# Kernel optimization log

Hardware: AMD Instinct MI355X
Metric: run time of the kernel (lower is better)

Reference implementation:

```python
import jax, jax.numpy as jnp
import numpy as np

B, C, K, P, STRIDE, ITERS = 32, 32, 3, 4, 1, 3
PSIZE = P * P
EPS = 1e-6


def unfold_patches(x, K, stride):
    # Replicates F.unfold(x_chw, kernel_size=K, padding=K//2, stride=stride)
    # followed by transpose(1,2).view(b, oh, ow, K*K, c) — including the
    # channel-major flat ordering that the view reinterprets.
    b, h, w, c = x.shape
    pad = K // 2
    xp = jnp.pad(jnp.transpose(x, (0, 3, 1, 2)), ((0, 0), (0, 0), (pad, pad), (pad, pad)))
    oh = (h + 2 * pad - K) // stride + 1
    ow = (w + 2 * pad - K) // stride + 1
    rows = []
    for ki in range(K):
        cols = []
        for kj in range(K):
            cols.append(xp[:, :, ki:ki + (oh - 1) * stride + 1:stride, kj:kj + (ow - 1) * stride + 1:stride])
        rows.append(jnp.stack(cols, axis=2))  # (b, c, K, oh, ow)
    pat = jnp.stack(rows, axis=2)  # (b, c, K, K, oh, ow)
    pat = pat.reshape(b, c * K * K, oh * ow)  # unfold output (b, c*K*K, L)
    pat = jnp.transpose(pat, (0, 2, 1)).reshape(b, oh, ow, K * K, c)
    return pat, oh, ow


def squash(s, eps=EPS):
    s2 = jnp.sum(s * s, axis=-1, keepdims=True)
    return (s2 / (1.0 + s2)) * s / jnp.sqrt(s2 + eps)


def dynamic_routing(v, a_in, iters=ITERS, eps=EPS):
    # v: (n, in_votes, C, psize), a_in: (n, in_votes, 1)
    n, in_votes, Cc, _ = v.shape
    b_ij = jnp.zeros((n, in_votes, Cc), dtype=v.dtype)
    a_in = jnp.clip(a_in, 0.0001, 1.0)
    v_j = None
    for t in range(iters):
        c_ij = jax.nn.softmax(b_ij, axis=2) * a_in
        c_ij = c_ij / (jnp.sum(c_ij, axis=2, keepdims=True) + eps)
        s_j = jnp.einsum('nic,nicq->ncq', c_ij, v)
        v_j = squash(s_j)
        if t < iters - 1:
            agreement = jnp.einsum('nicq,ncq->nic', v, v_j)
            b_ij = b_ij + agreement
    a_out = jnp.clip(jnp.sqrt(jnp.sum(v_j * v_j, axis=-1) + eps), 0.0001, 1.0 - 0.0001)
    return v_j, a_out


def setup_inputs() -> dict:
    key = jax.random.key(0)
    k1, k2 = jax.random.split(key)
    x = jax.random.normal(k1, (2, 14, 14, B * (PSIZE + 1)), dtype=jnp.float32)
    weights = jax.random.normal(k2, (K * K * B, C, PSIZE, PSIZE), dtype=jnp.float32) * 0.02
    return {"x": x, "weights": weights}


def reference(x, weights):
    b, h, w, c = x.shape
    patches, oh, ow = unfold_patches(x, K, STRIDE)
    p_in = patches[..., :B * PSIZE].reshape(b * oh * ow, K * K * B, PSIZE)
    a_in = patches[..., B * PSIZE:].reshape(b * oh * ow, K * K * B, 1)
    votes = jnp.einsum('bip,icpq->bicq', p_in, weights)  # (n, KKB, C, psize)
    p_vec, a_vec = dynamic_routing(votes, a_in)
    p_out = p_vec.reshape(b, oh, ow, C * PSIZE)
    a_out = a_vec.reshape(b, oh, ow, C)
    out = jnp.concatenate([p_out, a_out], axis=3)
    p_out = jnp.nan_to_num(p_out, nan=0.0, posinf=10000.0, neginf=-10000.0)
    a_out = jnp.nan_to_num(a_out, nan=0.5, posinf=1.0 - 0.0001, neginf=0.0001)
    out = jnp.nan_to_num(out, nan=0.0, posinf=10000.0, neginf=-10000.0)
    return p_out, a_out, out
```

## Files before the change

kernel.cpp:

```cpp
#include <hip/hip_runtime.h>
#include <hip/hip_fp16.h>
#include <math.h>

#define NB 392
#define NI 288
#define NC 32
#define NQ 16
#define CQ 512
#define CH 544
#define EPSV 1e-6f

#define VSCALE 32.0f
#define VINV (1.0f / 32.0f)

#define OFF_AOUT 200704
#define OFF_CAT  213248

#define RT_THREADS 512
#define RT_WAVES 8

typedef _Float16 v4h __attribute__((ext_vector_type(4)));
typedef float v4f __attribute__((ext_vector_type(4)));
typedef float v2f __attribute__((ext_vector_type(2)));

__device__ __forceinline__ float gather_x(const float* __restrict__ x, int n, int j) {
    int c_idx = j / 9;
    int rem = j - c_idx * 9;
    int ki = rem / 3;
    int kj = rem - ki * 3;
    int b_ = n / 196;
    int rest = n - b_ * 196;
    int yy = rest / 14;
    int xx = rest - yy * 14;
    int iy = yy + ki - 1;
    int ix = xx + kj - 1;
    float v = 0.f;
    if ((unsigned)iy < 14u && (unsigned)ix < 14u)
        v = x[((b_ * 14 + iy) * 14 + ix) * CH + c_idx];
    return v;
}

__global__ __launch_bounds__(256) void votes_k(const float* __restrict__ x,
                                               const float* __restrict__ wts,
                                               uchar* __restrict__ votes) {
    __shared__ uint tile[64 * 36];
    int mtt = blockIdx.x;
    int i = blockIdx.y;
    int t = threadIdx.x;
    int wv = t >> 6;
    int l = t & 63;
    int col = l & 15;
    int quad = l >> 4;

    int n_row = mtt * 64 + wv * 16 + col;
    v4h av = {};
    if (n_row < NB) {
        int jb = (i >> 5) * CH + (i & 31) * 16 + quad * 4;
#pragma unroll
        for (int kk = 0; kk < 4; ++kk)
            av[kk] = (_Float16)gather_x(x, n_row, jb + kk);
    }

    const float* wb = wts + (size_t)i * 8192 + quad * 64 + col;
    const uchar* tileb = (const uchar*)tile;

    for (int ch = 0; ch < 4; ++ch) {
#pragma unroll
        for (int c8 = 0; c8 < 8; ++c8) {
            int ct = ch * 8 + c8;
            const float* wp = wb + ct * 256;
            v4h bv;
            bv[0] = (_Float16)wp[0];
            bv[1] = (_Float16)wp[16];
            bv[2] = (_Float16)wp[32];
            bv[3] = (_Float16)wp[48];
            v4f acc = {0.f, 0.f, 0.f, 0.f};
            acc = __builtin_amdgcn_mfma_f32_16x16x16f16(bv, av, acc, 0, 0, 0);
            uint u = __builtin_amdgcn_cvt_pk_fp8_f32(acc[0] * VSCALE, acc[1] * VSCALE, 0, false);
            u = __builtin_amdgcn_cvt_pk_fp8_f32(acc[2] * VSCALE, acc[3] * VSCALE, u, true);
            tile[(wv * 16 + col) * 36 + c8 * 4 + quad] = u;
        }
        __syncthreads();
#pragma unroll
        for (int k = 0; k < 2; ++k) {
            int idx = k * 256 + t;
            int row = idx >> 3;
            int off = idx & 7;
            int n_out = mtt * 64 + row;
            if (n_out < NB) {
                uint4 d = *(const uint4*)&tileb[row * 144 + off * 16];
                *(uint4*)(votes + (((size_t)n_out * NI + i) << 9) + ch * 128 + off * 16) = d;
            }
        }
        __syncthreads();
    }
}

__global__ __launch_bounds__(RT_THREADS) void routing_k(const uchar* __restrict__ votes,
                                                        const float* __restrict__ x,
                                                        float* __restrict__ out) {
    __shared__ float afs[NI];
    __shared__ float sred[RT_WAVES * CQ];
    __shared__ float vj[CQ];
    __shared__ float aout_s[NC];

    int n = blockIdx.x;
    int t = threadIdx.x;
    int wv = t >> 6;
    int l = t & 63;
    int c = l & 31;
    int g = l >> 5;

    if (t < NI) {
        int j = (t >> 5) * CH + 512 + (t & 31);
        float v = gather_x(x, n, j);
        float a = fminf(fmaxf(v, 1e-4f), 1.0f);
        afs[t] = a / (a + EPSV);
    }
    __syncthreads();

    const uchar* vb = votes + (size_t)n * NI * 512;
    float vjr[16];
    float sreg[16];

#define VROW(S) (((const uint4*)(vb + ((size_t)(((((S) << 3) + wv) << 1) + g) << 9)))[c])

    for (int iter = 0; iter < 3; ++iter) {
#pragma unroll
        for (int q = 0; q < 16; ++q) sreg[q] = 0.f;

        uint4 f0 = VROW(0), f1 = VROW(1), f2 = VROW(2), f3 = VROW(3);

#pragma clang loop unroll_count(2)
        for (int s = 0; s < 18; ++s) {
            int i = ((s << 3) + wv) * 2 + g;
            uint4 cur = f0;
            f0 = f1; f1 = f2; f2 = f3;
            if (s + 4 < 18) f3 = VROW(s + 4);

            float vt[16];
            {
                v2f p;
                p = __builtin_amdgcn_cvt_pk_f32_fp8(cur.x, false); vt[0] = p[0];  vt[1] = p[1];
                p = __builtin_amdgcn_cvt_pk_f32_fp8(cur.x, true);  vt[2] = p[0];  vt[3] = p[1];
                p = __builtin_amdgcn_cvt_pk_f32_fp8(cur.y, false); vt[4] = p[0];  vt[5] = p[1];
                p = __builtin_amdgcn_cvt_pk_f32_fp8(cur.y, true);  vt[6] = p[0];  vt[7] = p[1];
                p = __builtin_amdgcn_cvt_pk_f32_fp8(cur.z, false); vt[8] = p[0];  vt[9] = p[1];
                p = __builtin_amdgcn_cvt_pk_f32_fp8(cur.z, true);  vt[10] = p[0]; vt[11] = p[1];
                p = __builtin_amdgcn_cvt_pk_f32_fp8(cur.w, false); vt[12] = p[0]; vt[13] = p[1];
                p = __builtin_amdgcn_cvt_pk_f32_fp8(cur.w, true);  vt[14] = p[0]; vt[15] = p[1];
            }
            float cij;
            if (iter == 0) {
                cij = afs[i] * (1.0f / 32.0f);
            } else {
                float ah = 0.f;
#pragma unroll
                for (int q = 0; q < 16; ++q) ah += vt[q] * vjr[q];
                float e = __expf(ah);
                float ssum = e;
                ssum += __shfl_xor(ssum, 1);
                ssum += __shfl_xor(ssum, 2);
                ssum += __shfl_xor(ssum, 4);
                ssum += __shfl_xor(ssum, 8);
                ssum += __shfl_xor(ssum, 16);
                cij = e * __builtin_amdgcn_rcpf(ssum) * afs[i];
            }
#pragma unroll
            for (int q = 0; q < 16; ++q) sreg[q] += cij * vt[q];
        }

#pragma unroll
        for (int q = 0; q < 16; ++q) sreg[q] += __shfl_xor(sreg[q], 32);
        if (g == 0) {
            float* sw = &sred[wv * CQ + c];
#pragma unroll
            for (int q = 0; q < 16; ++q) sw[q * 32] = sreg[q];
        }
        __syncthreads();
        {
            float ssum = 0.f;
#pragma unroll
            for (int k = 0; k < RT_WAVES; ++k) ssum += sred[k * CQ + t];
            sred[t] = ssum * VINV;
        }
        __syncthreads();

        if (t < NC) {
            float s2 = 0.f;
#pragma unroll
            for (int q = 0; q < 16; ++q) {
                float s = sred[q * 32 + t];
                s2 += s * s;
            }
            float f = (s2 / (1.f + s2)) / sqrtf(s2 + EPSV);
            float vn2 = 0.f;
#pragma unroll
            for (int q = 0; q < 16; ++q) {
                float v = f * sred[q * 32 + t];
                vj[q * 32 + t] = v;
                vn2 += v * v;
            }
            if (iter == 2) {
                float ao = sqrtf(vn2 + EPSV);
                ao = fminf(fmaxf(ao, 1e-4f), 1.f - 1e-4f);
                aout_s[t] = ao;
            }
        }
        __syncthreads();
        if (iter < 2) {
#pragma unroll
            for (int q = 0; q < 16; ++q) {
                float v = vj[q * 32 + c] * VINV;
                vjr[q] = (iter == 0) ? v : vjr[q] + v;
            }
        }
    }

    {
        float v = vj[(t & 15) * 32 + (t >> 4)];
        out[(size_t)n * CQ + t] = v;
        out[OFF_CAT + (size_t)n * 544 + t] = v;
    }
    if (t < NC) {
        float ao = aout_s[t];
        out[OFF_AOUT + n * 32 + t] = ao;
        out[OFF_CAT + (size_t)n * 544 + 512 + t] = ao;
    }
}

extern "C" void kernel_launch(void* const* d_in, const int* in_sizes, int n_in,
                              void* d_out, int out_size, void* d_ws, size_t ws_size,
                              hipStream_t stream) {
    const float* x = (const float*)d_in[0];
    const float* wts = (const float*)d_in[1];
    float* out = (float*)d_out;
    uchar* votes = (uchar*)d_ws;

    hipLaunchKernelGGL(votes_k, dim3(7, NI), dim3(256), 0, stream,
                       x, wts, votes);
    hipLaunchKernelGGL(routing_k, dim3(NB), dim3(RT_THREADS), 0, stream,
                       votes, x, out);
}
```

Baseline: 115.3 us.

## Cache per-capsule fp8 votes in LDS for later routing iterations

In the routing kernel, the first iteration writes each block's fp8 vote rows (288x512 bytes) into shared memory as it streams them from global memory. Iterations two and three then read votes from LDS instead of refetching them from global memory or L2. To fit the roughly 144KB cache, the cross-wave reduction buffer is halved and the reduction is split into two phases with an extra barrier. The block now uses almost all of the CU's LDS, which limits occupancy to one 512-thread block per CU.

```diff
diff --git a/kernel.cpp b/kernel.cpp
--- a/kernel.cpp
+++ b/kernel.cpp
@@ -17,7 +17,6 @@
 #define OFF_CAT  213248
 
 #define RT_THREADS 512
-#define RT_WAVES 8
 
 typedef _Float16 v4h __attribute__((ext_vector_type(4)));
 typedef float v4f __attribute__((ext_vector_type(4)));
@@ -99,9 +98,10 @@
 __global__ __launch_bounds__(RT_THREADS) void routing_k(const uchar* __restrict__ votes,
                                                         const float* __restrict__ x,
                                                         float* __restrict__ out) {
+    __shared__ uint4 vlds4[NI * 32];
+    __shared__ float sred[4 * CQ];
+    __shared__ float vj[CQ];
     __shared__ float afs[NI];
-    __shared__ float sred[RT_WAVES * CQ];
-    __shared__ float vj[CQ];
     __shared__ float aout_s[NC];
 
     int n = blockIdx.x;
@@ -125,63 +125,35 @@
 
 #define VROW(S) (((const uint4*)(vb + ((size_t)(((((S) << 3) + wv) << 1) + g) << 9)))[c])
 
-    for (int iter = 0; iter < 3; ++iter) {
-#pragma unroll
-        for (int q = 0; q < 16; ++q) sreg[q] = 0.f;
-
-        uint4 f0 = VROW(0), f1 = VROW(1), f2 = VROW(2), f3 = VROW(3);
-
-#pragma clang loop unroll_count(2)
-        for (int s = 0; s < 18; ++s) {
-            int i = ((s << 3) + wv) * 2 + g;
-            uint4 cur = f0;
-            f0 = f1; f1 = f2; f2 = f3;
-            if (s + 4 < 18) f3 = VROW(s + 4);
-
-            float vt[16];
-            {
-                v2f p;
-                p = __builtin_amdgcn_cvt_pk_f32_fp8(cur.x, false); vt[0] = p[0];  vt[1] = p[1];
-                p = __builtin_amdgcn_cvt_pk_f32_fp8(cur.x, true);  vt[2] = p[0];  vt[3] = p[1];
-                p = __builtin_amdgcn_cvt_pk_f32_fp8(cur.y, false); vt[4] = p[0];  vt[5] = p[1];
-                p = __builtin_amdgcn_cvt_pk_f32_fp8(cur.y, true);  vt[6] = p[0];  vt[7] = p[1];
-                p = __builtin_amdgcn_cvt_pk_f32_fp8(cur.z, false); vt[8] = p[0];  vt[9] = p[1];
-                p = __builtin_amdgcn_cvt_pk_f32_fp8(cur.z, true);  vt[10] = p[0]; vt[11] = p[1];
-                p = __builtin_amdgcn_cvt_pk_f32_fp8(cur.w, false); vt[12] = p[0]; vt[13] = p[1];
-                p = __builtin_amdgcn_cvt_pk_f32_fp8(cur.w, true);  vt[14] = p[0]; vt[15] = p[1];
-            }
-            float cij;
-            if (iter == 0) {
-                cij = afs[i] * (1.0f / 32.0f);
-            } else {
-                float ah = 0.f;
-#pragma unroll
-                for (int q = 0; q < 16; ++q) ah += vt[q] * vjr[q];
-                float e = __expf(ah);
-                float ssum = e;
-                ssum += __shfl_xor(ssum, 1);
-                ssum += __shfl_xor(ssum, 2);
-                ssum += __shfl_xor(ssum, 4);
-                ssum += __shfl_xor(ssum, 8);
-                ssum += __shfl_xor(ssum, 16);
-                cij = e * __builtin_amdgcn_rcpf(ssum) * afs[i];
-            }
-#pragma unroll
-            for (int q = 0; q < 16; ++q) sreg[q] += cij * vt[q];
-        }
-
+#define DECODE(CUR, VT) { v2f p_; \
+    p_ = __builtin_amdgcn_cvt_pk_f32_fp8(CUR.x, false); VT[0] = p_[0];  VT[1] = p_[1]; \
+    p_ = __builtin_amdgcn_cvt_pk_f32_fp8(CUR.x, true);  VT[2] = p_[0];  VT[3] = p_[1]; \
+    p_ = __builtin_amdgcn_cvt_pk_f32_fp8(CUR.y, false); VT[4] = p_[0];  VT[5] = p_[1]; \
+    p_ = __builtin_amdgcn_cvt_pk_f32_fp8(CUR.y, true);  VT[6] = p_[0];  VT[7] = p_[1]; \
+    p_ = __builtin_amdgcn_cvt_pk_f32_fp8(CUR.z, false); VT[8] = p_[0];  VT[9] = p_[1]; \
+    p_ = __builtin_amdgcn_cvt_pk_f32_fp8(CUR.z, true);  VT[10] = p_[0]; VT[11] = p_[1]; \
+    p_ = __builtin_amdgcn_cvt_pk_f32_fp8(CUR.w, false); VT[12] = p_[0]; VT[13] = p_[1]; \
+    p_ = __builtin_amdgcn_cvt_pk_f32_fp8(CUR.w, true);  VT[14] = p_[0]; VT[15] = p_[1]; }
+
+    auto reduce_squash = [&](int iter) {
 #pragma unroll
         for (int q = 0; q < 16; ++q) sreg[q] += __shfl_xor(sreg[q], 32);
-        if (g == 0) {
+        if (g == 0 && wv < 4) {
             float* sw = &sred[wv * CQ + c];
 #pragma unroll
             for (int q = 0; q < 16; ++q) sw[q * 32] = sreg[q];
+        }
+        __syncthreads();
+        if (g == 0 && wv >= 4) {
+            float* sw = &sred[(wv - 4) * CQ + c];
+#pragma unroll
+            for (int q = 0; q < 16; ++q) sw[q * 32] += sreg[q];
         }
         __syncthreads();
         {
             float ssum = 0.f;
 #pragma unroll
-            for (int k = 0; k < RT_WAVES; ++k) ssum += sred[k * CQ + t];
+            for (int k = 0; k < 4; ++k) ssum += sred[k * CQ + t];
             sred[t] = ssum * VINV;
         }
         __syncthreads();
@@ -215,6 +187,59 @@
                 vjr[q] = (iter == 0) ? v : vjr[q] + v;
             }
         }
+    };
+
+    {
+#pragma unroll
+        for (int q = 0; q < 16; ++q) sreg[q] = 0.f;
+
+        uint4 f0 = VROW(0), f1 = VROW(1), f2 = VROW(2), f3 = VROW(3);
+
+#pragma clang loop unroll_count(2)
+        for (int s = 0; s < 18; ++s) {
+            int i = (s << 4) + (wv << 1) + g;
+            uint4 cur = f0;
+            f0 = f1; f1 = f2; f2 = f3;
+            if (s + 4 < 18) f3 = VROW(s + 4);
+
+            vlds4[i * 32 + c] = cur;
+
+            float vt[16];
+            DECODE(cur, vt);
+            float cij = afs[i] * (1.0f / 32.0f);
+#pragma unroll
+            for (int q = 0; q < 16; ++q) sreg[q] += cij * vt[q];
+        }
+        reduce_squash(0);
+    }
+
+    for (int iter = 1; iter < 3; ++iter) {
+#pragma unroll
+        for (int q = 0; q < 16; ++q) sreg[q] = 0.f;
+
+#pragma clang loop unroll_count(2)
+        for (int s = 0; s < 18; ++s) {
+            int i = (s << 4) + (wv << 1) + g;
+            uint4 cur = vlds4[i * 32 + c];
+
+            float vt[16];
+            DECODE(cur, vt);
+
+            float ah = 0.f;
+#pragma unroll
+            for (int q = 0; q < 16; ++q) ah += vt[q] * vjr[q];
+            float e = __expf(ah);
+            float ssum = e;
+            ssum += __shfl_xor(ssum, 1);
+            ssum += __shfl_xor(ssum, 2);
+            ssum += __shfl_xor(ssum, 4);
+            ssum += __shfl_xor(ssum, 8);
+            ssum += __shfl_xor(ssum, 16);
+            float cij = e * __builtin_amdgcn_rcpf(ssum) * afs[i];
+#pragma unroll
+            for (int q = 0; q < 16; ++q) sreg[q] += cij * vt[q];
+        }
+        reduce_squash(iter);
     }
 
     {
```

After: 124.2 us. 1.08x slower.
